# Performance work log

Hardware: AMD Instinct MI355X
Metric: run time of the kernel (lower is better)

Reference implementation:

```python
import jax, jax.numpy as jnp
import numpy as np

LN_EPS = 1e-5


def setup_inputs() -> dict:
    key = jax.random.key(0)
    k_x, k_w = jax.random.split(key)
    B, T, F, M = 128, 512, 512, 512
    x = jax.random.normal(k_x, (B, T, F), dtype=jnp.float32)
    gamma = jnp.ones((T,), dtype=jnp.float32)
    beta = jnp.zeros((T,), dtype=jnp.float32)
    W = jax.random.normal(k_w, (M, T), dtype=jnp.float32) * 0.02  # Linear(T -> M) weight
    b = jnp.zeros((M,), dtype=jnp.float32)
    return {"x": x, "gamma": gamma, "beta": beta, "W": W, "b": b}


def reference(x, gamma, beta, W, b):
    # x: [B, T, F]. LayerNorm over the time axis T per (batch, feature) row,
    # matching norm(x.permute(0,2,1).reshape(-1, T)).
    mean = jnp.mean(x, axis=1, keepdims=True)                 # [B,1,F]
    var = jnp.mean((x - mean) ** 2, axis=1, keepdims=True)     # [B,1,F]
    xn = (x - mean) * jax.lax.rsqrt(var + LN_EPS)
    xn = xn * gamma[None, :, None] + beta[None, :, None]       # [B,T,F]
    # time_mlp: Linear along T (applied to [B,F,T] rows), output [B,F,M]
    # expressed directly in [B,T,F] layout -> [B,M,F]
    y = jnp.einsum('btf,mt->bmf', xn, W) + b[None, :, None]
    y = jax.nn.gelu(y, approximate=False)                      # torch nn.GELU is exact
    # dropout_prob = 0.0 -> identity; residual (M == T)
    return y + x
```

## Files before the change

kernel.cpp:

```cpp
#include <hip/hip_runtime.h>
#include <hip/hip_bf16.h>
#include <cstdint>


#define B_ 128
#define T_ 512
#define F_ 512
#define M_ 512
#define FT 32
#define XN_STRIDE 520

typedef __attribute__((ext_vector_type(8))) short bf16x8;
typedef __attribute__((ext_vector_type(4))) float f32x4;

static __device__ __forceinline__ unsigned short f2bf(float f) {
    unsigned int u = __float_as_uint(f);
    unsigned int r = u + 0x7FFFu + ((u >> 16) & 1u);
    return (unsigned short)(r >> 16);
}

static __device__ __forceinline__ void gld_lds16(const void* gptr, void* lptr) {
    __builtin_amdgcn_global_load_lds(
        (const __attribute__((address_space(1))) unsigned int*)gptr,
        (__attribute__((address_space(3))) unsigned int*)lptr,
        16, 0, 0);
}

__global__ void wconv_kernel(const float* __restrict__ W, unsigned short* __restrict__ Wb) {
    int i = (blockIdx.x * 256 + threadIdx.x) * 4;
    float4 v = *(const float4*)(W + i);
    ushort4 o;
    o.x = f2bf(v.x); o.y = f2bf(v.y); o.z = f2bf(v.z); o.w = f2bf(v.w);
    *(ushort4*)(Wb + i) = o;
}

__global__ __launch_bounds__(512, 4) void timemix_main(
    const float* __restrict__ x, const float* __restrict__ gamma,
    const float* __restrict__ beta, const unsigned short* __restrict__ Wb,
    const float* __restrict__ bias, float* __restrict__ out)
{
    __shared__ __align__(16) unsigned char smem[70400];
    unsigned char* xnS = smem;
    unsigned char* wS  = smem + 33280;
    float* red_sum = (float*)(smem + 33280);
    float* red_sq  = (float*)(smem + 33280 + 2048);
    float* gS      = (float*)(smem + 66048);
    float* bS      = (float*)(smem + 68096);
    float* meanS   = (float*)(smem + 70144);
    float* rstdS   = (float*)(smem + 70272);

    const int tid   = threadIdx.x;
    const int w     = tid >> 6;
    const int lane  = tid & 63;
    const int batch = blockIdx.y;
    const int f0    = blockIdx.x * FT;

    gS[tid] = gamma[tid];
    bS[tid] = beta[tid];

    const int f  = lane & 31;
    const int tg = w * 2 + (lane >> 5);
    float xv[32];
    {
        const float* xb = x + ((size_t)batch * T_ + (size_t)tg * 32) * F_ + f0 + f;
        float s = 0.f, q = 0.f;
        #pragma unroll
        for (int i = 0; i < 32; ++i) {
            float v = xb[(size_t)i * F_];
            xv[i] = v; s += v; q += v * v;
        }
        red_sum[tg * 32 + f] = s;
        red_sq [tg * 32 + f] = q;
    }
    __syncthreads();

    if (tid < 32) {
        float s = 0.f, q = 0.f;
        #pragma unroll
        for (int g = 0; g < 16; ++g) { s += red_sum[g * 32 + tid]; q += red_sq[g * 32 + tid]; }
        float mean = s * (1.0f / 512.0f);
        float var  = q * (1.0f / 512.0f) - mean * mean;
        meanS[tid] = mean;
        rstdS[tid] = rsqrtf(var + 1e-5f);
    }
    __syncthreads();

    {
        const float mean = meanS[f];
        const float rstd = rstdS[f];
        #pragma unroll
        for (int c = 0; c < 4; ++c) {
            const int t0 = tg * 32 + c * 8;
            unsigned int pr[4];
            #pragma unroll
            for (int h = 0; h < 4; ++h) {
                float a0 = rstd * gS[t0 + 2 * h];
                float v0 = xv[c * 8 + 2 * h] * a0 + (bS[t0 + 2 * h] - mean * a0);
                float a1 = rstd * gS[t0 + 2 * h + 1];
                float v1 = xv[c * 8 + 2 * h + 1] * a1 + (bS[t0 + 2 * h + 1] - mean * a1);
                pr[h] = (unsigned int)f2bf(v0) | ((unsigned int)f2bf(v1) << 16);
            }
            uint4 pk; pk.x = pr[0]; pk.y = pr[1]; pk.z = pr[2]; pk.w = pr[3];
            *(uint4*)(xnS + (size_t)f * (XN_STRIDE * 2) + t0 * 2) = pk;
        }
    }
    __syncthreads();

    const int lr = lane & 15;
    const int q4 = lane >> 4;
    f32x4 acc[4][2];
    #pragma unroll
    for (int mi = 0; mi < 4; ++mi)
        #pragma unroll
        for (int fi = 0; fi < 2; ++fi)
            acc[mi][fi] = (f32x4){0.f, 0.f, 0.f, 0.f};

    const int srow = lane >> 2;
    const int sch  = lane & 3;

    for (int kc = 0; kc < 16; ++kc) {
        const int k0 = kc * 32;
        __builtin_amdgcn_sched_barrier(0);
        #pragma unroll
        for (int r = 0; r < 4; ++r) {
            const int m0 = w * 64 + r * 16;
            const void* g = (const void*)(Wb + (size_t)(m0 + srow) * 512 + k0 + sch * 8);
            void* l = (void*)(wS + m0 * 64);
            gld_lds16(g, l);
        }
        __builtin_amdgcn_s_waitcnt(0x0F70);
        __builtin_amdgcn_sched_barrier(0);

        bf16x8 af[4], bfr[2];
        #pragma unroll
        for (int mi = 0; mi < 4; ++mi)
            af[mi] = *(const bf16x8*)(wS + (size_t)(w * 64 + mi * 16 + lr) * 64 + q4 * 16);
        #pragma unroll
        for (int fi = 0; fi < 2; ++fi)
            bfr[fi] = *(const bf16x8*)(xnS + (size_t)(fi * 16 + lr) * (XN_STRIDE * 2) + k0 * 2 + q4 * 16);
        #pragma unroll
        for (int mi = 0; mi < 4; ++mi)
            #pragma unroll
            for (int fi = 0; fi < 2; ++fi)
                acc[mi][fi] = __builtin_amdgcn_mfma_f32_16x16x32_bf16(af[mi], bfr[fi], acc[mi][fi], 0, 0, 0);
    }

    #pragma unroll
    for (int mi = 0; mi < 4; ++mi) {
        const int mbase = w * 64 + mi * 16 + q4 * 4;
        #pragma unroll
        for (int r = 0; r < 4; ++r) {
            const int m = mbase + r;
            const float bv = bias[m];
            #pragma unroll
            for (int fi = 0; fi < 2; ++fi) {
                float y = acc[mi][fi][r] + bv;
                float gl = 0.5f * y * (1.0f + erff(y * 0.70710678118654752f));
                size_t o = ((size_t)(batch * 512 + m)) * 512 + (size_t)(f0 + fi * 16 + lr);
                out[o] = gl + x[o];
            }
        }
    }
}

extern "C" void kernel_launch(void* const* d_in, const int* in_sizes, int n_in,
                              void* d_out, int out_size, void* d_ws, size_t ws_size,
                              hipStream_t stream) {
    const float* x     = (const float*)d_in[0];
    const float* gamma = (const float*)d_in[1];
    const float* beta  = (const float*)d_in[2];
    const float* W     = (const float*)d_in[3];
    const float* bias  = (const float*)d_in[4];
    float* out = (float*)d_out;
    unsigned short* Wb = (unsigned short*)d_ws;

    wconv_kernel<<<dim3(M_ * T_ / (256 * 4)), 256, 0, stream>>>(W, Wb);
    dim3 grid(F_ / FT, B_);
    timemix_main<<<grid, 512, 0, stream>>>(x, gamma, beta, Wb, bias, out);
}
```

Measured before the change: 322.8 us.

## Pre-swizzle W into MFMA fragment order and load A fragments directly to registers

The weight conversion kernel now writes bf16 W in the exact per-lane MFMA fragment order, so each lane can load its A operand with one 16-byte global load. This drops the LDS staging of W and its waitcnt stalls. The main loop double-buffers the A fragments in registers across k-chunks. LDS use per block falls from about 70 KB to about 41 KB, which may allow more resident blocks per CU, but the W reads now depend on L2/L1 hits from every wave.

Result: faster. 303.8 us (-5.9%).

```diff
diff --git a/kernel.cpp b/kernel.cpp
--- a/kernel.cpp
+++ b/kernel.cpp
@@ -19,35 +19,37 @@
     return (unsigned short)(r >> 16);
 }
 
-static __device__ __forceinline__ void gld_lds16(const void* gptr, void* lptr) {
-    __builtin_amdgcn_global_load_lds(
-        (const __attribute__((address_space(1))) unsigned int*)gptr,
-        (__attribute__((address_space(3))) unsigned int*)lptr,
-        16, 0, 0);
-}
-
-__global__ void wconv_kernel(const float* __restrict__ W, unsigned short* __restrict__ Wb) {
-    int i = (blockIdx.x * 256 + threadIdx.x) * 4;
-    float4 v = *(const float4*)(W + i);
-    ushort4 o;
-    o.x = f2bf(v.x); o.y = f2bf(v.y); o.z = f2bf(v.z); o.w = f2bf(v.w);
-    *(ushort4*)(Wb + i) = o;
+__global__ void wconv_kernel(const float* __restrict__ W, unsigned short* __restrict__ Wq) {
+    int idx  = blockIdx.x * 256 + threadIdx.x;
+    int lane = idx & 63;
+    int mg   = (idx >> 6) & 31;
+    int kc   = idx >> 11;
+    int m = mg * 16 + (lane & 15);
+    int k = kc * 32 + (lane >> 4) * 8;
+    const float* src = W + (size_t)m * 512 + k;
+    float4 v0 = *(const float4*)(src);
+    float4 v1 = *(const float4*)(src + 4);
+    uint4 o;
+    o.x = (unsigned int)f2bf(v0.x) | ((unsigned int)f2bf(v0.y) << 16);
+    o.y = (unsigned int)f2bf(v0.z) | ((unsigned int)f2bf(v0.w) << 16);
+    o.z = (unsigned int)f2bf(v1.x) | ((unsigned int)f2bf(v1.y) << 16);
+    o.w = (unsigned int)f2bf(v1.z) | ((unsigned int)f2bf(v1.w) << 16);
+    *(uint4*)(Wq + (size_t)idx * 8) = o;
 }
 
 __global__ __launch_bounds__(512, 4) void timemix_main(
     const float* __restrict__ x, const float* __restrict__ gamma,
-    const float* __restrict__ beta, const unsigned short* __restrict__ Wb,
+    const float* __restrict__ beta, const unsigned short* __restrict__ Wq,
     const float* __restrict__ bias, float* __restrict__ out)
 {
-    __shared__ __align__(16) unsigned char smem[70400];
+    __shared__ __align__(16) unsigned char smem[37632];
     unsigned char* xnS = smem;
-    unsigned char* wS  = smem + 33280;
-    float* red_sum = (float*)(smem + 33280);
-    float* red_sq  = (float*)(smem + 33280 + 2048);
-    float* gS      = (float*)(smem + 66048);
-    float* bS      = (float*)(smem + 68096);
-    float* meanS   = (float*)(smem + 70144);
-    float* rstdS   = (float*)(smem + 70272);
+    float* gS    = (float*)(smem + 33280);
+    float* bS    = (float*)(smem + 35328);
+    float* meanS = (float*)(smem + 37376);
+    float* rstdS = (float*)(smem + 37504);
+    __shared__ float red_sum[16 * 32];
+    __shared__ float red_sq[16 * 32];
 
     const int tid   = threadIdx.x;
     const int w     = tid >> 6;
@@ -108,6 +110,8 @@
 
     const int lr = lane & 15;
     const int q4 = lane >> 4;
+    const unsigned short* wbase = Wq + ((size_t)(w * 4) * 64 + lane) * 8;
+
     f32x4 acc[4][2];
     #pragma unroll
     for (int mi = 0; mi < 4; ++mi)
@@ -115,34 +119,38 @@
         for (int fi = 0; fi < 2; ++fi)
             acc[mi][fi] = (f32x4){0.f, 0.f, 0.f, 0.f};
 
-    const int srow = lane >> 2;
-    const int sch  = lane & 3;
+    bf16x8 aA[4], aB[4];
+    #pragma unroll
+    for (int mi = 0; mi < 4; ++mi)
+        aA[mi] = *(const bf16x8*)(wbase + (size_t)mi * 512);
 
-    for (int kc = 0; kc < 16; ++kc) {
-        const int k0 = kc * 32;
-        __builtin_amdgcn_sched_barrier(0);
-        #pragma unroll
-        for (int r = 0; r < 4; ++r) {
-            const int m0 = w * 64 + r * 16;
-            const void* g = (const void*)(Wb + (size_t)(m0 + srow) * 512 + k0 + sch * 8);
-            void* l = (void*)(wS + m0 * 64);
-            gld_lds16(g, l);
-        }
-        __builtin_amdgcn_s_waitcnt(0x0F70);
-        __builtin_amdgcn_sched_barrier(0);
-
-        bf16x8 af[4], bfr[2];
+    for (int kc = 0; kc < 16; kc += 2) {
         #pragma unroll
         for (int mi = 0; mi < 4; ++mi)
-            af[mi] = *(const bf16x8*)(wS + (size_t)(w * 64 + mi * 16 + lr) * 64 + q4 * 16);
-        #pragma unroll
-        for (int fi = 0; fi < 2; ++fi)
-            bfr[fi] = *(const bf16x8*)(xnS + (size_t)(fi * 16 + lr) * (XN_STRIDE * 2) + k0 * 2 + q4 * 16);
-        #pragma unroll
-        for (int mi = 0; mi < 4; ++mi)
+            aB[mi] = *(const bf16x8*)(wbase + (size_t)(kc + 1) * 16384 + (size_t)mi * 512);
+        {
+            bf16x8 b0 = *(const bf16x8*)(xnS + (size_t)lr * (XN_STRIDE * 2) + kc * 64 + q4 * 16);
+            bf16x8 b1 = *(const bf16x8*)(xnS + (size_t)(16 + lr) * (XN_STRIDE * 2) + kc * 64 + q4 * 16);
             #pragma unroll
-            for (int fi = 0; fi < 2; ++fi)
-                acc[mi][fi] = __builtin_amdgcn_mfma_f32_16x16x32_bf16(af[mi], bfr[fi], acc[mi][fi], 0, 0, 0);
+            for (int mi = 0; mi < 4; ++mi) {
+                acc[mi][0] = __builtin_amdgcn_mfma_f32_16x16x32_bf16(aA[mi], b0, acc[mi][0], 0, 0, 0);
+                acc[mi][1] = __builtin_amdgcn_mfma_f32_16x16x32_bf16(aA[mi], b1, acc[mi][1], 0, 0, 0);
+            }
+        }
+        if (kc + 2 < 16) {
+            #pragma unroll
+            for (int mi = 0; mi < 4; ++mi)
+                aA[mi] = *(const bf16x8*)(wbase + (size_t)(kc + 2) * 16384 + (size_t)mi * 512);
+        }
+        {
+            bf16x8 b0 = *(const bf16x8*)(xnS + (size_t)lr * (XN_STRIDE * 2) + (kc + 1) * 64 + q4 * 16);
+            bf16x8 b1 = *(const bf16x8*)(xnS + (size_t)(16 + lr) * (XN_STRIDE * 2) + (kc + 1) * 64 + q4 * 16);
+            #pragma unroll
+            for (int mi = 0; mi < 4; ++mi) {
+                acc[mi][0] = __builtin_amdgcn_mfma_f32_16x16x32_bf16(aB[mi], b0, acc[mi][0], 0, 0, 0);
+                acc[mi][1] = __builtin_amdgcn_mfma_f32_16x16x32_bf16(aB[mi], b1, acc[mi][1], 0, 0, 0);
+            }
+        }
     }
 
     #pragma unroll
@@ -172,9 +180,9 @@
     const float* W     = (const float*)d_in[3];
     const float* bias  = (const float*)d_in[4];
     float* out = (float*)d_out;
-    unsigned short* Wb = (unsigned short*)d_ws;
+    unsigned short* Wq = (unsigned short*)d_ws;
 
-    wconv_kernel<<<dim3(M_ * T_ / (256 * 4)), 256, 0, stream>>>(W, Wb);
+    wconv_kernel<<<dim3(128), 256, 0, stream>>>(W, Wq);
     dim3 grid(F_ / FT, B_);
-    timemix_main<<<grid, 512, 0, stream>>>(x, gamma, beta, Wb, bias, out);
+    timemix_main<<<grid, 512, 0, stream>>>(x, gamma, beta, Wq, bias, out);
 }
```
